# Performance work log

Hardware: AMD Instinct MI355X
Metric: run time of the kernel (lower is better)

## Reference

```python
import math
import jax, jax.numpy as jnp
import numpy as np

NUM_BINS = 36
TOP_K = 8
HIDDEN = 256
B, Q = 16, 900
TWO_PI = 2.0 * math.pi
BIN_SIZE = TWO_PI / NUM_BINS
BIG = 1e9  # finite stand-in for +inf in masked sorts (avoids inf-inf NaNs)


def _circ_dist(a, b):
    # torch: min(|a-b|, 2pi-|a-b|).clamp(max=pi/2)  (upper clamp only)
    diff = jnp.abs(a - b)
    return jnp.minimum(jnp.minimum(diff, TWO_PI - diff), math.pi / 2)


def _masked_quantile(vals, mask, n):
    # torch.quantile(vals[mask], q) with q = 1 - 1/(n+1), linear interpolation.
    s = jnp.sort(jnp.where(mask, vals, BIG))  # valid entries first
    nf = n.astype(vals.dtype)
    q = 1.0 - 1.0 / (nf + 1.0)
    pos = q * jnp.maximum(nf - 1.0, 0.0)
    M = vals.shape[0]
    lo = jnp.clip(jnp.floor(pos).astype(jnp.int32), 0, M - 1)
    hi = jnp.clip(jnp.ceil(pos).astype(jnp.int32), 0, M - 1)
    frac = pos - lo.astype(vals.dtype)
    return s[lo] + (s[hi] - s[lo]) * frac


def _per_batch(qf, pa, W):
    Qn = qf.shape[0]
    angles = jnp.arctan2(pa[:, 1], pa[:, 0]) % TWO_PI            # [Q]
    bins = jnp.clip((angles / BIN_SIZE).astype(jnp.int32), 0, NUM_BINS - 1)
    fused = qf + W[bins]
    nq = fused / jnp.maximum(jnp.linalg.norm(fused, axis=-1, keepdims=True), 1e-12)
    sim = nq @ nq.T                                              # [Q,Q]
    sim = jnp.where(jnp.eye(Qn, dtype=bool), -jnp.inf, sim)

    iu, ju = np.triu_indices(Qn, 1)                              # static, i<j
    i_idx = jnp.asarray(iu, jnp.int32); j_idx = jnp.asarray(ju, jnp.int32)
    p_sim = sim[i_idx, j_idx]                                    # [P]
    bi, bj = bins[i_idx], bins[j_idx]
    seg = jnp.minimum(bi, bj) * NUM_BINS + jnp.maximum(bi, bj)   # canonical bin-pair id
    NB2 = NUM_BINS * NUM_BINS
    P = p_sim.shape[0]

    # per-bin-pair argmax (first-occurrence, matching torch.argmax order)
    seg_max = jax.ops.segment_max(jax.lax.stop_gradient(p_sim), seg, num_segments=NB2)
    seg_cnt = jax.ops.segment_sum(jnp.ones((P,), jnp.int32), seg, num_segments=NB2)
    cand = jnp.where(p_sim == seg_max[seg], jnp.arange(P, dtype=jnp.int32), P)
    sel = jnp.clip(jax.ops.segment_min(cand, seg, num_segments=NB2), 0, P - 1)  # [NB2]
    valid = seg_cnt > 0
    sel_sim = p_sim[sel]

    # quantile filter over selected pairs
    S = valid.sum()
    thr = _masked_quantile(sel_sim, valid, S)
    mask1 = valid & (sel_sim > thr)

    # top-k fallback over all off-diagonal sims (Q^2-Q >= TOP_K always here)
    th2 = jax.lax.top_k(sim.reshape(-1), TOP_K)[0][-1]
    use_fb = mask1.sum() < 2
    maskF = jnp.where(use_fb, valid & (sel_sim >= th2), mask1)
    cnt = maskF.sum()

    ai = angles[i_idx[sel]]; aj = angles[j_idx[sel]]
    d = _circ_dist(ai, aj)
    # torch.median: lower-middle order statistic at index (n-1)//2
    ds = jnp.sort(jnp.where(maskF, d, BIG))
    med = ds[jnp.clip((cnt - 1) // 2, 0, NB2 - 1)]
    alpha = jnp.clip(med, math.pi / NUM_BINS, math.pi / 2)
    coop_m = maskF & (d <= alpha)
    comp_m = maskF & (d > alpha)

    # cooperative loss: pull angles toward circular mean of each pair
    mean_ang = jnp.arctan2((jnp.sin(ai) + jnp.sin(aj)) * 0.5,
                           (jnp.cos(ai) + jnp.cos(aj)) * 0.5)
    l_coop = _circ_dist(ai, mean_ang) ** 2 + _circ_dist(aj, mean_ang) ** 2
    n_coop = coop_m.sum()
    coop_b = jnp.sum(jnp.where(coop_m, l_coop, 0.0)) / jnp.maximum(n_coop, 1)

    # competitive loss: squared hinge above quantile margin of comp sims
    n_comp = comp_m.sum()
    margin = _masked_quantile(sel_sim, comp_m, n_comp)
    viol = jnp.maximum(sel_sim - margin, 0.0)
    comp_b = jnp.sum(jnp.where(comp_m, viol * viol, 0.0)) / jnp.maximum(n_comp, 1)

    return coop_b, comp_b, cnt > 0


def setup_inputs() -> dict:
    key = jax.random.key(0)
    k1, k2, k3 = jax.random.split(key, 3)
    return {
        "query_features": jax.random.normal(k1, (B, Q, HIDDEN), dtype=jnp.float32),
        "predicted_angles": jax.random.normal(k2, (B, Q, 2), dtype=jnp.float32),
        "bin_embeddings": jax.random.normal(k3, (NUM_BINS, HIDDEN), dtype=jnp.float32) * 0.02,
    }


def reference(query_features, predicted_angles, bin_embeddings):
    coop, comp, vb = jax.vmap(_per_batch, in_axes=(0, 0, None))(
        query_features, predicted_angles, bin_embeddings)
    denom = jnp.maximum(vb.sum(), 1)
    return (coop.sum() / denom, comp.sum() / denom)
```

## Files before the change

### kernel.cpp

```cpp
#include <hip/hip_runtime.h>
#include <math.h>

typedef unsigned int u32;
typedef unsigned long long u64;
typedef unsigned short ushortT;
typedef __attribute__((ext_vector_type(8))) short short8;
typedef __attribute__((ext_vector_type(4))) float f32x4;

#define Qn    900
#define Bn    16
#define Hn    256
#define NBINS 36
#define NB2   1296
#define T64   64
#define NTILE64 15
#define NP64  120
#define NSLOT 6
#define PS    ((size_t)Bn * Qn * Hn)
#define TWO_PI_F 6.2831853071795864769f
#define PI_F     3.1415926535897932385f
#define HALF_PI_F 1.5707963267948966f
#define BIN_SIZE_F (TWO_PI_F / 36.0f)
#define BIGV 1e9f

__device__ __forceinline__ u32 fkey(float f) {
    u32 u = __float_as_uint(f);
    return (u & 0x80000000u) ? ~u : (u | 0x80000000u);
}
__device__ __forceinline__ float unfkey(u32 k) {
    u32 u = (k & 0x80000000u) ? (k ^ 0x80000000u) : ~k;
    return __uint_as_float(u);
}
__device__ __forceinline__ float circdist(float a, float b) {
    float diff = fabsf(a - b);
    return fminf(fminf(diff, TWO_PI_F - diff), HALF_PI_F);
}
__device__ __forceinline__ void ins4(float* t4, float v) {
    if (v > t4[3]) {
        if (v > t4[0]) { t4[3]=t4[2]; t4[2]=t4[1]; t4[1]=t4[0]; t4[0]=v; }
        else if (v > t4[1]) { t4[3]=t4[2]; t4[2]=t4[1]; t4[1]=v; }
        else if (v > t4[2]) { t4[3]=t4[2]; t4[2]=v; }
        else t4[3]=v;
    }
}
__device__ __forceinline__ void ins2(float& m1, float& m2, float x) {
    if (x > m1) { m2 = m1; m1 = x; }
    else if (x > m2) m2 = x;
}
__device__ __forceinline__ ushortT bf16rne(float x, float& back) {
    u32 u = __float_as_uint(x);
    u32 r = u + 0x7FFFu + ((u >> 16) & 1u);
    ushortT h = (ushortT)(r >> 16);
    back = __uint_as_float(((u32)h) << 16);
    return h;
}
__device__ __forceinline__ void gl_lds16(const ushortT* g, ushortT* l) {
    __builtin_amdgcn_global_load_lds(
        (const __attribute__((address_space(1))) unsigned int*)g,
        (__attribute__((address_space(3))) unsigned int*)l,
        16, 0, 0);
}

__device__ __forceinline__ int bSumI(int v, volatile int* red) {
    #pragma unroll
    for (int off = 32; off >= 1; off >>= 1) v += __shfl_xor(v, off, 64);
    int w = threadIdx.x >> 6;
    if ((threadIdx.x & 63) == 0) red[w] = v;
    __syncthreads();
    int r = red[0] + red[1] + red[2] + red[3];
    __syncthreads();
    return r;
}
__device__ __forceinline__ float bSumF(float v, volatile float* red) {
    #pragma unroll
    for (int off = 32; off >= 1; off >>= 1) v += __shfl_xor(v, off, 64);
    int w = threadIdx.x >> 6;
    if ((threadIdx.x & 63) == 0) red[w] = v;
    __syncthreads();
    float r = red[0] + red[1] + red[2] + red[3];
    __syncthreads();
    return r;
}
__device__ __forceinline__ u32 bMinU(u32 v, volatile u32* red) {
    #pragma unroll
    for (int off = 32; off >= 1; off >>= 1) {
        u32 o = (u32)__shfl_xor((int)v, off, 64);
        v = v < o ? v : o;
    }
    int w = threadIdx.x >> 6;
    if ((threadIdx.x & 63) == 0) red[w] = v;
    __syncthreads();
    u32 r = red[0];
    if (red[1] < r) r = red[1];
    if (red[2] < r) r = red[2];
    if (red[3] < r) r = red[3];
    __syncthreads();
    return r;
}
__device__ __forceinline__ void bTop2(float m1, float m2, volatile float* red2,
                                      float& o1, float& o2) {
    #pragma unroll
    for (int off = 32; off >= 1; off >>= 1) {
        float a1 = __shfl_xor(m1, off, 64);
        float a2 = __shfl_xor(m2, off, 64);
        ins2(m1, m2, a1); ins2(m1, m2, a2);
    }
    int w = threadIdx.x >> 6;
    if ((threadIdx.x & 63) == 0) { red2[w * 2] = m1; red2[w * 2 + 1] = m2; }
    __syncthreads();
    float r1 = red2[0], r2 = red2[1];
    #pragma unroll
    for (int ww = 1; ww < 4; ww++) { ins2(r1, r2, red2[ww * 2]); ins2(r1, r2, red2[ww * 2 + 1]); }
    __syncthreads();
    o1 = r1; o2 = r2;
}
__device__ u32 selRank(const u32* ckeys, int m, int p, volatile u32* redU) {
    u32 best = 0xFFFFFFFFu;
    for (int base = 0; base < m; base += 256) {
        int idx = base + (int)threadIdx.x;
        if (idx < m) {
            u32 k = ckeys[idx];
            int c = 0;
            for (int j = 0; j < m; j++) c += (ckeys[j] <= k);
            if (c >= p + 1 && k < best) best = k;
        }
    }
    return bMinU(best, redU);
}
__device__ __forceinline__ float quantTop2(float top1, float top2, int n) {
    float nf = (float)n;
    float qq = 1.f - 1.f / (nf + 1.f);
    float pos = qq * fmaxf(nf - 1.f, 0.f);
    int lo = (int)floorf(pos), hi = (int)ceilf(pos);
    float frac = pos - (float)lo;
    float slo = (lo >= n - 1) ? top1 : top2;
    float shi = (hi >= n - 1) ? top1 : top2;
    return slo + (shi - slo) * frac;
}

__global__ void k0_sort(const float* __restrict__ pa, float* __restrict__ anglesO,
                        int* __restrict__ binsO, int* __restrict__ sortPos,
                        int* __restrict__ origIdx, int* __restrict__ binSorted,
                        u64* __restrict__ segBest, u32* __restrict__ bcnt) {
    int b = blockIdx.x, t = threadIdx.x;
    __shared__ int hist[NBINS], offs[NBINS], offs2[NBINS];
    if (t < NBINS) hist[t] = 0;
    if (b == 0 && t < (Bn + 1)) bcnt[t * 16] = 0u;
    for (int s = t; s < NB2; s += 256) segBest[(size_t)b * NB2 + s] = 0ULL;
    __syncthreads();
    for (int q = t; q < Qn; q += blockDim.x) {
        float x = pa[(b * Qn + q) * 2 + 0];
        float y = pa[(b * Qn + q) * 2 + 1];
        float a = atan2f(y, x);
        if (a < 0.f) a += TWO_PI_F;
        int bin = (int)(a / BIN_SIZE_F);
        bin = bin < 0 ? 0 : (bin > NBINS - 1 ? NBINS - 1 : bin);
        anglesO[b * Qn + q] = a;
        binsO[b * Qn + q] = bin;
        atomicAdd(&hist[bin], 1);
    }
    __syncthreads();
    if (t == 0) { int s = 0; for (int i = 0; i < NBINS; i++) { offs[i] = s; s += hist[i]; } }
    __syncthreads();
    if (t < NBINS) offs2[t] = offs[t];
    __syncthreads();
    for (int q = t; q < Qn; q += blockDim.x) {
        int bin = binsO[b * Qn + q];
        int pos = atomicAdd(&offs2[bin], 1);
        sortPos[b * Qn + q] = pos;
        origIdx[b * Qn + pos] = q;
        binSorted[b * Qn + pos] = bin;
    }
}

__global__ void k1_norm(const float4* __restrict__ qf, const float4* __restrict__ W,
                        const int* __restrict__ binsO, const int* __restrict__ sortPos,
                        ushortT* __restrict__ nqB) {
    int b = blockIdx.x;
    int w = threadIdx.x >> 6, lane = threadIdx.x & 63;
    int q = blockIdx.y * 4 + w;
    int bin = binsO[b * Qn + q];
    float4 v = qf[(size_t)(b * Qn + q) * (Hn / 4) + lane];
    float4 wv = W[(size_t)bin * (Hn / 4) + lane];
    v.x += wv.x; v.y += wv.y; v.z += wv.z; v.w += wv.w;
    float ss = v.x * v.x + v.y * v.y + v.z * v.z + v.w * v.w;
    #pragma unroll
    for (int off = 32; off >= 1; off >>= 1) ss += __shfl_xor(ss, off, 64);
    float sc = 1.f / fmaxf(sqrtf(ss), 1e-12f);
    float xs[4] = {v.x * sc, v.y * sc, v.z * sc, v.w * sc};
    ushort4 p0, p1;
    ushortT* h0 = (ushortT*)&p0; ushortT* h1 = (ushortT*)&p1;
    #pragma unroll
    for (int c = 0; c < 4; c++) {
        float f0, f1;
        h0[c] = bf16rne(xs[c], f0);
        float r1 = xs[c] - f0;
        h1[c] = bf16rne(r1, f1);
    }
    int sp = sortPos[b * Qn + q];
    size_t base = ((size_t)(b * Qn + sp)) * Hn + lane * 4;
    *(ushort4*)(nqB + 0 * PS + base) = p0;
    *(ushort4*)(nqB + 1 * PS + base) = p1;
}

__global__ __launch_bounds__(256, 4) void k2_gemm(
        const ushortT* __restrict__ nqB, const int* __restrict__ binSorted,
        const int* __restrict__ origIdx, u64* __restrict__ segBest,
        float* __restrict__ topCand, const float* __restrict__ anglesO,
        float* __restrict__ batchRes, u32* __restrict__ bcnt,
        float* __restrict__ out) {
    __shared__ __align__(16) union Sh {
        ushortT stage[4 * 2048];
        u64     segLds[NB2];
        u32     ckeys[NB2];
    } sh;
    __shared__ int rbins[T64], cbins[T64], rois[T64], cois[T64];
    __shared__ float t4w[16];
    __shared__ int redI[4];
    __shared__ float redF[4];
    __shared__ u32 redU[4];
    __shared__ float red2[8];
    __shared__ int mcnt, shLast;
    __shared__ float sth2;

    int lin = blockIdx.x;
    int xcd = lin & 7;
    int slot = lin >> 3;
    int b = xcd * 2 + (slot >= NP64 ? 1 : 0);
    int tp = (slot >= NP64) ? slot - NP64 : slot;
    int ti = 0, rem = tp;
    while (rem >= NTILE64 - ti) { rem -= NTILE64 - ti; ti++; }
    int tj = ti + rem;
    int rowBase = ti * T64, colBase = tj * T64;
    int t = threadIdx.x;
    int w = t >> 6, lane = t & 63;
    int wrow = w >> 1, wcol = w & 1;
    int lq = lane >> 4, lm = lane & 15;

    if (t < T64) {
        int sr = rowBase + t, sc = colBase + t;
        rbins[t] = (sr < Qn) ? binSorted[b * Qn + sr] : 0;
        rois[t]  = (sr < Qn) ? origIdx[b * Qn + sr] : 0;
        cbins[t] = (sc < Qn) ? binSorted[b * Qn + sc] : 0;
        cois[t]  = (sc < Qn) ? origIdx[b * Qn + sc] : 0;
    }

    f32x4 acc[2][2];
    #pragma unroll
    for (int i = 0; i < 2; i++)
        #pragma unroll
        for (int j = 0; j < 2; j++) acc[i][j] = (f32x4){0.f, 0.f, 0.f, 0.f};

    u32 goff[4];
    int loff[4];
    #pragma unroll
    for (int i = 0; i < 4; i++) {
        int p = i & 1;
        int sideB = i >> 1;
        int row = t >> 2;
        int udata = (t & 3) ^ ((t >> 3) & 3);
        int gq = (sideB ? colBase : rowBase) + row;
        if (gq >= Qn) gq = Qn - 1;
        goff[i] = (u32)(p * (u32)PS) + (u32)(b * Qn + gq) * Hn + (u32)(udata * 8);
        loff[i] = i * 2048 + t * 8;
    }
    int aswz = (lq ^ ((lm >> 1) & 3)) * 8;

    for (int kc = 0; kc < Hn; kc += 32) {
        #pragma unroll
        for (int i = 0; i < 4; i++)
            gl_lds16(nqB + goff[i] + kc, &sh.stage[loff[i]]);
        __syncthreads();

        short8 af[2][2];
        #pragma unroll
        for (int p = 0; p < 2; p++)
            #pragma unroll
            for (int mt = 0; mt < 2; mt++)
                af[p][mt] = *(const short8*)&sh.stage[p * 2048 + (wrow * 32 + mt * 16 + lm) * 32 + aswz];

        #pragma unroll
        for (int nt = 0; nt < 2; nt++) {
            int coff = (wcol * 32 + nt * 16 + lm) * 32 + aswz;
            short8 b0 = *(const short8*)&sh.stage[2 * 2048 + coff];
            short8 b1 = *(const short8*)&sh.stage[3 * 2048 + coff];
            #pragma unroll
            for (int mt = 0; mt < 2; mt++) {
                f32x4 c = acc[mt][nt];
                c = __builtin_amdgcn_mfma_f32_16x16x32_bf16(af[0][mt], b0, c, 0, 0, 0);
                c = __builtin_amdgcn_mfma_f32_16x16x32_bf16(af[0][mt], b1, c, 0, 0, 0);
                c = __builtin_amdgcn_mfma_f32_16x16x32_bf16(af[1][mt], b0, c, 0, 0, 0);
                c = __builtin_amdgcn_mfma_f32_16x16x32_bf16(af[1][mt], b1, c, 0, 0, 0);
                acc[mt][nt] = c;
            }
        }
        __syncthreads();
    }

    for (int s = t; s < NB2; s += 256) sh.segLds[s] = 0ULL;
    __syncthreads();

    float t4[4] = {-3e38f, -3e38f, -3e38f, -3e38f};
    int curSeg = -1; u64 curBest = 0ULL;
    #pragma unroll
    for (int mt = 0; mt < 2; mt++) {
        #pragma unroll
        for (int r = 0; r < 4; r++) {
            int lrr = wrow * 32 + mt * 16 + lq * 4 + r;
            int sr = rowBase + lrr;
            int bi = rbins[lrr], io = rois[lrr];
            #pragma unroll
            for (int nt = 0; nt < 2; nt++) {
                int lcc = wcol * 32 + nt * 16 + lm;
                int sc = colBase + lcc;
                bool ok = (sr < Qn) && (sc < Qn) && (sr < sc);
                if (ok) {
                    float v = acc[mt][nt][r];
                    ins4(t4, v);
                    int bj = cbins[lcc], jo = cois[lcc];
                    int bmin = bi < bj ? bi : bj, bmax = bi < bj ? bj : bi;
                    int seg = bmin * NBINS + bmax;
                    int imin = io < jo ? io : jo, jmax = io < jo ? jo : io;
                    u64 packed = ((u64)fkey(v) << 32) | (u32)(~(((u32)imin << 10) | (u32)jmax));
                    if (seg == curSeg) { if (packed > curBest) curBest = packed; }
                    else {
                        if (curSeg >= 0) atomicMax(&sh.segLds[curSeg], curBest);
                        curSeg = seg; curBest = packed;
                    }
                }
            }
        }
    }
    if (curSeg >= 0) atomicMax(&sh.segLds[curSeg], curBest);

    #pragma unroll
    for (int off = 32; off >= 1; off >>= 1) {
        float o0 = __shfl_xor(t4[0], off, 64);
        float o1 = __shfl_xor(t4[1], off, 64);
        float o2 = __shfl_xor(t4[2], off, 64);
        float o3 = __shfl_xor(t4[3], off, 64);
        ins4(t4, o0); ins4(t4, o1); ins4(t4, o2); ins4(t4, o3);
    }
    if (lane == 0) {
        t4w[w * 4 + 0] = t4[0]; t4w[w * 4 + 1] = t4[1];
        t4w[w * 4 + 2] = t4[2]; t4w[w * 4 + 3] = t4[3];
    }
    __syncthreads();

    for (int s = t; s < NB2; s += 256) {
        u64 v = sh.segLds[s];
        if (v) atomicMax(&segBest[(size_t)b * NB2 + s], v);
    }
    if (t == 0) {
        #pragma unroll
        for (int ww = 1; ww < 4; ww++) {
            ins4(t4, t4w[ww * 4 + 0]); ins4(t4, t4w[ww * 4 + 1]);
            ins4(t4, t4w[ww * 4 + 2]); ins4(t4, t4w[ww * 4 + 3]);
        }
        float* dst = topCand + (size_t)(b * NP64 + tp) * 4;
        #pragma unroll
        for (int c = 0; c < 4; c++)
            __hip_atomic_store(&dst[c], t4[c], __ATOMIC_RELAXED, __HIP_MEMORY_SCOPE_AGENT);
    }

    __syncthreads();
    if (t == 0) {
        u32 done = __hip_atomic_fetch_add(&bcnt[b * 16], 1u, __ATOMIC_RELAXED,
                                          __HIP_MEMORY_SCOPE_AGENT);
        shLast = (done == NP64 - 1) ? 1 : 0;
    }
    __syncthreads();
    if (!shLast) return;

    float rval[NSLOT], rd[NSLOT];
    u32 rcode[NSLOT];
    bool rvalid[NSLOT], rmF[NSLOT];
    #pragma unroll
    for (int k = 0; k < NSLOT; k++) {
        int s = t + k * 256;
        rvalid[k] = false; rval[k] = 0.f; rd[k] = 0.f; rcode[k] = 0u; rmF[k] = false;
        if (s < NB2) {
            u64 p = __hip_atomic_load(&segBest[(size_t)b * NB2 + s],
                                      __ATOMIC_RELAXED, __HIP_MEMORY_SCOPE_AGENT);
            if (p != 0ULL) {
                rvalid[k] = true;
                rval[k] = unfkey((u32)(p >> 32));
                rcode[k] = ~((u32)p);
                int i = (rcode[k] >> 10) & 1023, j = rcode[k] & 1023;
                float ai = anglesO[b * Qn + i], aj = anglesO[b * Qn + j];
                rd[k] = circdist(ai, aj);
            }
        }
    }

    int Sv = 0;
    float m1 = -3e38f, m2 = -3e38f;
    #pragma unroll
    for (int k = 0; k < NSLOT; k++)
        if (rvalid[k]) { Sv++; ins2(m1, m2, rval[k]); }
    int S = bSumI(Sv, redI);
    float top1, top2v;
    bTop2(m1, m2, red2, top1, top2v);
    float thr = (S == 0) ? BIGV : quantTop2(top1, top2v, S);

    int c1v = 0;
    #pragma unroll
    for (int k = 0; k < NSLOT; k++)
        if (rvalid[k] && rval[k] > thr) c1v++;
    int c1 = bSumI(c1v, redI);

    if (t < 64) {
        float t4l[4] = {-3e38f, -3e38f, -3e38f, -3e38f};
        for (int i = t; i < NP64 * 4; i += 64)
            ins4(t4l, __hip_atomic_load(&topCand[(size_t)b * NP64 * 4 + i],
                                        __ATOMIC_RELAXED, __HIP_MEMORY_SCOPE_AGENT));
        #pragma unroll
        for (int off = 32; off >= 1; off >>= 1) {
            float o0 = __shfl_xor(t4l[0], off, 64);
            float o1 = __shfl_xor(t4l[1], off, 64);
            float o2 = __shfl_xor(t4l[2], off, 64);
            float o3 = __shfl_xor(t4l[3], off, 64);
            ins4(t4l, o0); ins4(t4l, o1); ins4(t4l, o2); ins4(t4l, o3);
        }
        if (t == 0) sth2 = t4l[3];
    }
    __syncthreads();
    float th2 = sth2;

    bool use_fb = (c1 < 2);
    int cv = 0;
    #pragma unroll
    for (int k = 0; k < NSLOT; k++) {
        bool mF = use_fb ? (rvalid[k] && rval[k] >= th2)
                         : (rvalid[k] && rval[k] > thr);
        rmF[k] = mF;
        cv += mF ? 1 : 0;
    }
    int cnt = bSumI(cv, redI);

    if (t == 0) mcnt = 0;
    __syncthreads();
    #pragma unroll
    for (int k = 0; k < NSLOT; k++) {
        bool pred = rmF[k];
        u32 key = fkey(rd[k]);
        u64 bal = __ballot(pred);
        int prefix = __popcll(bal & ((1ULL << lane) - 1ULL));
        int tot = __popcll(bal);
        int base = 0;
        if (lane == 0) base = tot ? atomicAdd(&mcnt, tot) : 0;
        base = __shfl(base, 0, 64);
        if (pred) sh.ckeys[base + prefix] = key;
    }
    __syncthreads();
    int m2c = mcnt;

    float med;
    if (cnt == 0) med = BIGV;
    else {
        int midx = (cnt - 1) >> 1;
        med = unfkey(selRank(sh.ckeys, m2c, midx, redU));
    }
    float alpha = fminf(fmaxf(med, PI_F / (float)NBINS), HALF_PI_F);

    int ncoopv = 0, ncompv = 0; float coopv = 0.f;
    float c1m = -3e38f, c2m = -3e38f;
    #pragma unroll
    for (int k = 0; k < NSLOT; k++) {
        if (!rmF[k]) continue;
        if (rd[k] <= alpha) {
            ncoopv++;
            int i = (rcode[k] >> 10) & 1023, j = rcode[k] & 1023;
            float ai = anglesO[b * Qn + i], aj = anglesO[b * Qn + j];
            float mm = atan2f((sinf(ai) + sinf(aj)) * 0.5f, (cosf(ai) + cosf(aj)) * 0.5f);
            float d1 = circdist(ai, mm), d2 = circdist(aj, mm);
            coopv += d1 * d1 + d2 * d2;
        } else {
            ncompv++;
            ins2(c1m, c2m, rval[k]);
        }
    }
    int ncoop = bSumI(ncoopv, redI);
    float coopSum = bSumF(coopv, redF);
    int ncomp = bSumI(ncompv, redI);
    float ct1, ct2;
    bTop2(c1m, c2m, red2, ct1, ct2);
    float margin = (ncomp == 0) ? BIGV : quantTop2(ct1, ct2, ncomp);

    float compv = 0.f;
    #pragma unroll
    for (int k = 0; k < NSLOT; k++) {
        if (rmF[k] && rd[k] > alpha) {
            float viol = fmaxf(rval[k] - margin, 0.f);
            compv += viol * viol;
        }
    }
    float compSum = bSumF(compv, redF);

    if (t == 0) {
        float r0 = coopSum / (float)(ncoop > 1 ? ncoop : 1);
        float r1 = compSum / (float)(ncomp > 1 ? ncomp : 1);
        float r2 = cnt > 0 ? 1.f : 0.f;
        __hip_atomic_store(&batchRes[b * 3 + 0], r0, __ATOMIC_RELAXED, __HIP_MEMORY_SCOPE_AGENT);
        __hip_atomic_store(&batchRes[b * 3 + 1], r1, __ATOMIC_RELAXED, __HIP_MEMORY_SCOPE_AGENT);
        __hip_atomic_store(&batchRes[b * 3 + 2], r2, __ATOMIC_RELAXED, __HIP_MEMORY_SCOPE_AGENT);
        u32 doneB = __hip_atomic_fetch_add(&bcnt[Bn * 16], 1u, __ATOMIC_ACQ_REL,
                                           __HIP_MEMORY_SCOPE_AGENT);
        if (doneB == Bn - 1) {
            float cs = 0.f, ps = 0.f, vs = 0.f;
            for (int bb = 0; bb < Bn; bb++) {
                cs += __hip_atomic_load(&batchRes[bb * 3 + 0], __ATOMIC_RELAXED, __HIP_MEMORY_SCOPE_AGENT);
                ps += __hip_atomic_load(&batchRes[bb * 3 + 1], __ATOMIC_RELAXED, __HIP_MEMORY_SCOPE_AGENT);
                vs += __hip_atomic_load(&batchRes[bb * 3 + 2], __ATOMIC_RELAXED, __HIP_MEMORY_SCOPE_AGENT);
            }
            float denom = fmaxf(vs, 1.f);
            out[0] = cs / denom;
            out[1] = ps / denom;
        }
    }
}

extern "C" void kernel_launch(void* const* d_in, const int* in_sizes, int n_in,
                              void* d_out, int out_size, void* d_ws, size_t ws_size,
                              hipStream_t stream) {
    (void)in_sizes; (void)n_in; (void)out_size; (void)ws_size;
    const float* qf = (const float*)d_in[0];
    const float* pa = (const float*)d_in[1];
    const float* W  = (const float*)d_in[2];
    float* out = (float*)d_out;

    char* ws = (char*)d_ws;
    size_t off = 0;
    ushortT* nqB = (ushortT*)(ws + off);  off += 2 * PS * 2;
    float* anglesO = (float*)(ws + off);  off += (size_t)Bn * Qn * 4;
    int* binsO = (int*)(ws + off);        off += (size_t)Bn * Qn * 4;
    int* sortPos = (int*)(ws + off);      off += (size_t)Bn * Qn * 4;
    int* origIdx = (int*)(ws + off);      off += (size_t)Bn * Qn * 4;
    int* binSorted = (int*)(ws + off);    off += (size_t)Bn * Qn * 4;
    u64* segBest = (u64*)(ws + off);      off += (size_t)Bn * NB2 * 8;
    float* topCand = (float*)(ws + off);  off += (size_t)Bn * NP64 * 4 * 4;
    float* batchRes = (float*)(ws + off); off += (size_t)Bn * 3 * 4;
    u32* bcnt = (u32*)(ws + off);         off += (Bn + 1) * 64;

    k0_sort<<<Bn, 256, 0, stream>>>(pa, anglesO, binsO, sortPos, origIdx, binSorted,
                                    segBest, bcnt);
    k1_norm<<<dim3(Bn, 225), 256, 0, stream>>>((const float4*)qf, (const float4*)W,
                                               binsO, sortPos, nqB);
    k2_gemm<<<NP64 * Bn, 256, 0, stream>>>(nqB, binSorted, origIdx, segBest, topCand,
                                           anglesO, batchRes, bcnt, out);
}
```

Measured before the change: 138.8 us.

## Drop bin sort kernel and fuse angle/bin computation into normalization kernel

Removes the per-batch counting-sort kernel and computes angles and bins inside the normalization kernel, which now writes normalized rows in original query order. The GEMM epilogue uses original row and column indices directly for tie-breaking, so the origIdx and sortPos indirections go away. This saves one launch and a serial, low-parallelism 16-block kernel. In exchange, rows are no longer grouped by bin, so bin-pair segments change more often within a thread's outputs and cause more shared-memory 64-bit atomicMax calls in the epilogue.

Result: faster. 124.8 us (-10.1%).

```diff
diff --git a/kernel.cpp b/kernel.cpp
--- a/kernel.cpp
+++ b/kernel.cpp
@@ -138,48 +138,31 @@
     return slo + (shi - slo) * frac;
 }
 
-__global__ void k0_sort(const float* __restrict__ pa, float* __restrict__ anglesO,
-                        int* __restrict__ binsO, int* __restrict__ sortPos,
-                        int* __restrict__ origIdx, int* __restrict__ binSorted,
+__global__ void k1_prep(const float4* __restrict__ qf, const float4* __restrict__ W,
+                        const float* __restrict__ pa, float* __restrict__ anglesO,
+                        int* __restrict__ binsO, ushortT* __restrict__ nqB,
                         u64* __restrict__ segBest, u32* __restrict__ bcnt) {
-    int b = blockIdx.x, t = threadIdx.x;
-    __shared__ int hist[NBINS], offs[NBINS], offs2[NBINS];
-    if (t < NBINS) hist[t] = 0;
-    if (b == 0 && t < (Bn + 1)) bcnt[t * 16] = 0u;
-    for (int s = t; s < NB2; s += 256) segBest[(size_t)b * NB2 + s] = 0ULL;
-    __syncthreads();
-    for (int q = t; q < Qn; q += blockDim.x) {
-        float x = pa[(b * Qn + q) * 2 + 0];
-        float y = pa[(b * Qn + q) * 2 + 1];
-        float a = atan2f(y, x);
-        if (a < 0.f) a += TWO_PI_F;
-        int bin = (int)(a / BIN_SIZE_F);
-        bin = bin < 0 ? 0 : (bin > NBINS - 1 ? NBINS - 1 : bin);
+    int b = blockIdx.x;
+    int t = threadIdx.x;
+    int w = t >> 6, lane = t & 63;
+    int q = blockIdx.y * 4 + w;
+
+    if (blockIdx.y == 0) {
+        for (int s = t; s < NB2; s += 256) segBest[(size_t)b * NB2 + s] = 0ULL;
+        if (b == 0 && t < (Bn + 1)) bcnt[t * 16] = 0u;
+    }
+
+    float x = pa[(b * Qn + q) * 2 + 0];
+    float y = pa[(b * Qn + q) * 2 + 1];
+    float a = atan2f(y, x);
+    if (a < 0.f) a += TWO_PI_F;
+    int bin = (int)(a / BIN_SIZE_F);
+    bin = bin < 0 ? 0 : (bin > NBINS - 1 ? NBINS - 1 : bin);
+    if (lane == 0) {
         anglesO[b * Qn + q] = a;
         binsO[b * Qn + q] = bin;
-        atomicAdd(&hist[bin], 1);
-    }
-    __syncthreads();
-    if (t == 0) { int s = 0; for (int i = 0; i < NBINS; i++) { offs[i] = s; s += hist[i]; } }
-    __syncthreads();
-    if (t < NBINS) offs2[t] = offs[t];
-    __syncthreads();
-    for (int q = t; q < Qn; q += blockDim.x) {
-        int bin = binsO[b * Qn + q];
-        int pos = atomicAdd(&offs2[bin], 1);
-        sortPos[b * Qn + q] = pos;
-        origIdx[b * Qn + pos] = q;
-        binSorted[b * Qn + pos] = bin;
-    }
-}
-
-__global__ void k1_norm(const float4* __restrict__ qf, const float4* __restrict__ W,
-                        const int* __restrict__ binsO, const int* __restrict__ sortPos,
-                        ushortT* __restrict__ nqB) {
-    int b = blockIdx.x;
-    int w = threadIdx.x >> 6, lane = threadIdx.x & 63;
-    int q = blockIdx.y * 4 + w;
-    int bin = binsO[b * Qn + q];
+    }
+
     float4 v = qf[(size_t)(b * Qn + q) * (Hn / 4) + lane];
     float4 wv = W[(size_t)bin * (Hn / 4) + lane];
     v.x += wv.x; v.y += wv.y; v.z += wv.z; v.w += wv.w;
@@ -197,24 +180,22 @@
         float r1 = xs[c] - f0;
         h1[c] = bf16rne(r1, f1);
     }
-    int sp = sortPos[b * Qn + q];
-    size_t base = ((size_t)(b * Qn + sp)) * Hn + lane * 4;
+    size_t base = ((size_t)(b * Qn + q)) * Hn + lane * 4;
     *(ushort4*)(nqB + 0 * PS + base) = p0;
     *(ushort4*)(nqB + 1 * PS + base) = p1;
 }
 
 __global__ __launch_bounds__(256, 4) void k2_gemm(
-        const ushortT* __restrict__ nqB, const int* __restrict__ binSorted,
-        const int* __restrict__ origIdx, u64* __restrict__ segBest,
-        float* __restrict__ topCand, const float* __restrict__ anglesO,
-        float* __restrict__ batchRes, u32* __restrict__ bcnt,
-        float* __restrict__ out) {
+        const ushortT* __restrict__ nqB, const int* __restrict__ binsO,
+        u64* __restrict__ segBest, float* __restrict__ topCand,
+        const float* __restrict__ anglesO, float* __restrict__ batchRes,
+        u32* __restrict__ bcnt, float* __restrict__ out) {
     __shared__ __align__(16) union Sh {
         ushortT stage[4 * 2048];
         u64     segLds[NB2];
         u32     ckeys[NB2];
     } sh;
-    __shared__ int rbins[T64], cbins[T64], rois[T64], cois[T64];
+    __shared__ int rbins[T64], cbins[T64];
     __shared__ float t4w[16];
     __shared__ int redI[4];
     __shared__ float redF[4];
@@ -239,10 +220,8 @@
 
     if (t < T64) {
         int sr = rowBase + t, sc = colBase + t;
-        rbins[t] = (sr < Qn) ? binSorted[b * Qn + sr] : 0;
-        rois[t]  = (sr < Qn) ? origIdx[b * Qn + sr] : 0;
-        cbins[t] = (sc < Qn) ? binSorted[b * Qn + sc] : 0;
-        cois[t]  = (sc < Qn) ? origIdx[b * Qn + sc] : 0;
+        rbins[t] = (sr < Qn) ? binsO[b * Qn + sr] : 0;
+        cbins[t] = (sc < Qn) ? binsO[b * Qn + sc] : 0;
     }
 
     f32x4 acc[2][2];
@@ -308,7 +287,7 @@
         for (int r = 0; r < 4; r++) {
             int lrr = wrow * 32 + mt * 16 + lq * 4 + r;
             int sr = rowBase + lrr;
-            int bi = rbins[lrr], io = rois[lrr];
+            int bi = rbins[lrr];
             #pragma unroll
             for (int nt = 0; nt < 2; nt++) {
                 int lcc = wcol * 32 + nt * 16 + lm;
@@ -317,11 +296,10 @@
                 if (ok) {
                     float v = acc[mt][nt][r];
                     ins4(t4, v);
-                    int bj = cbins[lcc], jo = cois[lcc];
+                    int bj = cbins[lcc];
                     int bmin = bi < bj ? bi : bj, bmax = bi < bj ? bj : bi;
                     int seg = bmin * NBINS + bmax;
-                    int imin = io < jo ? io : jo, jmax = io < jo ? jo : io;
-                    u64 packed = ((u64)fkey(v) << 32) | (u32)(~(((u32)imin << 10) | (u32)jmax));
+                    u64 packed = ((u64)fkey(v) << 32) | (u32)(~(((u32)sr << 10) | (u32)sc));
                     if (seg == curSeg) { if (packed > curBest) curBest = packed; }
                     else {
                         if (curSeg >= 0) atomicMax(&sh.segLds[curSeg], curBest);
@@ -534,18 +512,13 @@
     ushortT* nqB = (ushortT*)(ws + off);  off += 2 * PS * 2;
     float* anglesO = (float*)(ws + off);  off += (size_t)Bn * Qn * 4;
     int* binsO = (int*)(ws + off);        off += (size_t)Bn * Qn * 4;
-    int* sortPos = (int*)(ws + off);      off += (size_t)Bn * Qn * 4;
-    int* origIdx = (int*)(ws + off);      off += (size_t)Bn * Qn * 4;
-    int* binSorted = (int*)(ws + off);    off += (size_t)Bn * Qn * 4;
     u64* segBest = (u64*)(ws + off);      off += (size_t)Bn * NB2 * 8;
     float* topCand = (float*)(ws + off);  off += (size_t)Bn * NP64 * 4 * 4;
     float* batchRes = (float*)(ws + off); off += (size_t)Bn * 3 * 4;
     u32* bcnt = (u32*)(ws + off);         off += (Bn + 1) * 64;
 
-    k0_sort<<<Bn, 256, 0, stream>>>(pa, anglesO, binsO, sortPos, origIdx, binSorted,
-                                    segBest, bcnt);
-    k1_norm<<<dim3(Bn, 225), 256, 0, stream>>>((const float4*)qf, (const float4*)W,
-                                               binsO, sortPos, nqB);
-    k2_gemm<<<NP64 * Bn, 256, 0, stream>>>(nqB, binSorted, origIdx, segBest, topCand,
+    k1_prep<<<dim3(Bn, 225), 256, 0, stream>>>((const float4*)qf, (const float4*)W,
+                                               pa, anglesO, binsO, nqB, segBest, bcnt);
+    k2_gemm<<<NP64 * Bn, 256, 0, stream>>>(nqB, binsO, segBest, topCand,
                                            anglesO, batchRes, bcnt, out);
 }
```
